# Kernel optimization log

Hardware: AMD Instinct MI355X
Metric: run time of the kernel (lower is better)

## Reference

```python
import jax, jax.numpy as jnp
import numpy as np

N_NODES = 100_000
N_EDGES = 800_000
IN_DIM = 128
OUT_DIM = 128
H = 8
D = OUT_DIM // H  # head dim = 16
SCALE = float(np.sqrt(OUT_DIM / H))


def setup_inputs() -> dict:
    key = jax.random.key(0)
    k1, k2, k3, k4, k5 = jax.random.split(key, 5)
    x = jax.random.normal(k1, (N_NODES, IN_DIM), dtype=jnp.float32)
    i_node = jax.random.randint(k2, (N_EDGES,), 0, N_NODES)
    j_node = jax.random.randint(k3, (N_EDGES,), 0, N_NODES)
    # nn.Linear weights (bias=False): [out_features, in_features]
    Wqkv = jax.random.normal(k4, (3 * OUT_DIM, IN_DIM), dtype=jnp.float32) / np.sqrt(IN_DIM)
    Wprj = jax.random.normal(k5, (OUT_DIM, OUT_DIM), dtype=jnp.float32) / np.sqrt(OUT_DIM)
    return {"x": x, "Wqkv": Wqkv, "Wprj": Wprj, "i_node": i_node, "j_node": j_node}


def reference(x, Wqkv, Wprj, i_node, j_node):
    N = x.shape[0]
    # node_tf_qkv then einops 'n (h d3) -> h n d3'; we keep [N, H, 3D] layout
    qkv = (x @ Wqkv.T).reshape(N, H, 3 * D)
    q, k, v = qkv[..., :D], qkv[..., D:2 * D], qkv[..., 2 * D:]  # chunk(dim=-1)
    q_e = q[i_node]   # [E, H, D] gather target-node queries
    k_e = k[j_node]   # [E, H, D] gather source-node keys
    v_e = v[j_node]   # [E, H, D] gather source-node values
    alpha = (q_e * k_e).sum(-1) / SCALE          # [E, H] per-edge scores
    # segment softmax grouped by target node i_node (torch_geometric softmax)
    m = jax.ops.segment_max(alpha, i_node, num_segments=N)      # [N, H]
    m = jnp.where(jnp.isfinite(m), m, 0.0)                      # nodes with no edges
    ex = jnp.exp(alpha - m[i_node])                             # [E, H]
    denom = jax.ops.segment_sum(ex, i_node, num_segments=N)     # [N, H]
    w = ex / (denom[i_node] + 1e-16)                            # [E, H]
    # scatter-add weighted values back to target nodes
    out = jax.ops.segment_sum(v_e * w[..., None], i_node, num_segments=N)  # [N, H, D]
    out = out.reshape(N, H * D)                  # einops 'h n d -> n (h d)'
    return out @ Wprj.T
```

## Files before the change

kernel.cpp:

```cpp
#include <hip/hip_runtime.h>
#include <hip/hip_bf16.h>
#include <math.h>

#define N_NODES 100000
#define N_EDGES 800000
#define CAP     64

typedef __bf16 bf16x8 __attribute__((ext_vector_type(8)));
typedef float  f32x4  __attribute__((ext_vector_type(4)));

__device__ inline unsigned short f2bf(float f) {
    unsigned u = __float_as_uint(f);
    u += 0x7FFF + ((u >> 16) & 1);
    return (unsigned short)(u >> 16);
}
__device__ inline float bflo(unsigned u) { return __uint_as_float(u << 16); }
__device__ inline float bfhi(unsigned u) { return __uint_as_float(u & 0xFFFF0000u); }
__device__ inline float2 bfpair(unsigned u) { return make_float2(bflo(u), bfhi(u)); }

__global__ __launch_bounds__(256) void cvt_weights(
    const float* __restrict__ wqkv, const float* __restrict__ wprj,
    unsigned short* __restrict__ wqkvbf, unsigned short* __restrict__ wprjbf)
{
    int idx = blockIdx.x * 256 + threadIdx.x;
    if (idx < 12288) {
        int r = idx >> 5, c4 = idx & 31;
        int h = r / 48, rem = r - h * 48;
        int part = rem >> 4, d = rem & 15;
        int nr = part * 128 + h * 16 + d;
        float4 v = ((const float4*)wqkv)[idx];
        ushort4 o;
        o.x = f2bf(v.x); o.y = f2bf(v.y); o.z = f2bf(v.z); o.w = f2bf(v.w);
        ((ushort4*)wqkvbf)[(nr << 5) + c4] = o;
    } else {
        int i = idx - 12288;
        float4 v = ((const float4*)wprj)[i];
        ushort4 o;
        o.x = f2bf(v.x); o.y = f2bf(v.y); o.z = f2bf(v.z); o.w = f2bf(v.w);
        ((ushort4*)wprjbf)[i] = o;
    }
}

template<bool AFP32, bool BF16OUT>
__global__ __launch_bounds__(256) void gemm_mfma(
    const void* __restrict__ Av, int M,
    const unsigned short* __restrict__ B,
    void* __restrict__ C, int Nb)
{
    __shared__ unsigned short As[64][136];
    __shared__ unsigned short Bs[64][136];
    const int t = threadIdx.x;
    const int row0 = blockIdx.x * 64;

    #pragma unroll
    for (int u = 0; u < 4; ++u) {
        int idx = t + u * 256;
        int r = idx >> 4, c = idx & 15;
        int gr = row0 + r;
        if (AFP32) {
            const float* ap = (const float*)Av + (size_t)gr * 128 + c * 8;
            float4 a0 = make_float4(0.f, 0.f, 0.f, 0.f), a1 = a0;
            if (gr < M) { a0 = ((const float4*)ap)[0]; a1 = ((const float4*)ap)[1]; }
            unsigned w0 = (unsigned)f2bf(a0.x) | ((unsigned)f2bf(a0.y) << 16);
            unsigned w1 = (unsigned)f2bf(a0.z) | ((unsigned)f2bf(a0.w) << 16);
            unsigned w2 = (unsigned)f2bf(a1.x) | ((unsigned)f2bf(a1.y) << 16);
            unsigned w3 = (unsigned)f2bf(a1.z) | ((unsigned)f2bf(a1.w) << 16);
            *(uint4*)&As[r][c * 8] = make_uint4(w0, w1, w2, w3);
        } else {
            float4 val = make_float4(0.f, 0.f, 0.f, 0.f);
            if (gr < M)
                val = *(const float4*)((const unsigned short*)Av + (size_t)gr * 128 + c * 8);
            *(float4*)&As[r][c * 8] = val;
        }
    }

    const int wid = t >> 6, lane = t & 63;
    const int wm = wid >> 1, wn = wid & 1;
    const int lrow = lane & 15, kg = lane >> 4;
    const int br = t >> 4, bc = (t & 15) * 8;

    float4 pb[4];
    #pragma unroll
    for (int u = 0; u < 4; ++u)
        pb[u] = *(const float4*)(B + (size_t)(br + u * 16) * 128 + bc);

    const int NT = Nb / 64;
    for (int ct = 0; ct < NT; ++ct) {
        __syncthreads();
        #pragma unroll
        for (int u = 0; u < 4; ++u)
            *(float4*)&Bs[br + u * 16][bc] = pb[u];
        if (ct + 1 < NT) {
            #pragma unroll
            for (int u = 0; u < 4; ++u)
                pb[u] = *(const float4*)(B + (size_t)((ct + 1) * 64 + br + u * 16) * 128 + bc);
        }
        __syncthreads();

        f32x4 acc[2][2] = {};
        #pragma unroll
        for (int ks = 0; ks < 4; ++ks) {
            bf16x8 af[2], bfr[2];
            #pragma unroll
            for (int m = 0; m < 2; ++m)
                af[m] = *(const bf16x8*)&As[wm * 32 + m * 16 + lrow][ks * 32 + kg * 8];
            #pragma unroll
            for (int n = 0; n < 2; ++n)
                bfr[n] = *(const bf16x8*)&Bs[wn * 32 + n * 16 + lrow][ks * 32 + kg * 8];
            #pragma unroll
            for (int m = 0; m < 2; ++m)
                #pragma unroll
                for (int n = 0; n < 2; ++n)
                    acc[m][n] = __builtin_amdgcn_mfma_f32_16x16x32_bf16(
                        af[m], bfr[n], acc[m][n], 0, 0, 0);
        }

        #pragma unroll
        for (int m = 0; m < 2; ++m)
            #pragma unroll
            for (int reg = 0; reg < 4; ++reg) {
                int gr = row0 + wm * 32 + m * 16 + kg * 4 + reg;
                if (gr < M) {
                    #pragma unroll
                    for (int n = 0; n < 2; ++n) {
                        int gc = ct * 64 + wn * 32 + n * 16 + lrow;
                        if (BF16OUT)
                            ((unsigned short*)C)[(size_t)gr * Nb + gc] = f2bf(acc[m][n][reg]);
                        else
                            ((float*)C)[(size_t)gr * Nb + gc] = acc[m][n][reg];
                    }
                }
            }
    }
}

__global__ __launch_bounds__(256) void scatter_cap(
    const int* __restrict__ i_node, const int* __restrict__ j_node,
    unsigned* __restrict__ cnt, int* __restrict__ jlist)
{
    int e = blockIdx.x * 256 + threadIdx.x;
    if (e < N_EDGES) {
        int i = i_node[e];
        unsigned pos = atomicAdd(&cnt[i], 1u);
        jlist[(size_t)i * CAP + pos] = j_node[e] * 384;
    }
}

__global__ __launch_bounds__(256) void node_gather(
    const unsigned short* __restrict__ qkv,
    const unsigned* __restrict__ cnt,
    const int* __restrict__ jlist,
    unsigned short* __restrict__ accum)
{
    int n = blockIdx.x * 4 + (threadIdx.x >> 6);
    if (n >= N_NODES) return;
    int lane = threadIdx.x & 63;
    int slot = lane >> 4, r = lane & 15;

    const uint4 q = *(const uint4*)(qkv + (size_t)n * 384 + r * 8);
    float2 qf[4] = { bfpair(q.x), bfpair(q.y), bfpair(q.z), bfpair(q.w) };

    unsigned deg = cnt[n];
    const int* jrow = jlist + (size_t)n * CAP;

    float2 acc[4] = {};
    float dsum = 0.f;
    for (unsigned it = 0; it < deg; it += 4) {
        unsigned idx = it + (unsigned)slot;
        bool act = idx < deg;
        int jb = jrow[act ? idx : 0];
        const unsigned short* kb = qkv + (size_t)jb + 128 + r * 8;
        uint4 kq = *(const uint4*)kb;
        uint4 vq = *(const uint4*)(kb + 128);
        float2 kf0 = bfpair(kq.x), kf1 = bfpair(kq.y), kf2 = bfpair(kq.z), kf3 = bfpair(kq.w);
        float2 d2 = qf[0] * kf0 + qf[1] * kf1 + qf[2] * kf2 + qf[3] * kf3;
        float ah = d2.x + d2.y;
        ah += __shfl_xor(ah, 1);
        float ex = act ? __expf(ah * 0.25f) : 0.f;
        dsum += ex;
        float2 e2 = make_float2(ex, ex);
        acc[0] += bfpair(vq.x) * e2;
        acc[1] += bfpair(vq.y) * e2;
        acc[2] += bfpair(vq.z) * e2;
        acc[3] += bfpair(vq.w) * e2;
    }

    float* af = (float*)acc;
    #pragma unroll
    for (int off = 16; off < 64; off <<= 1) {
        dsum += __shfl_xor(dsum, off);
        #pragma unroll
        for (int i = 0; i < 8; ++i) af[i] += __shfl_xor(af[i], off);
    }

    if (slot == 0) {
        float rs = 1.0f / (dsum + 1e-16f);
        unsigned o0 = (unsigned)f2bf(acc[0].x * rs) | ((unsigned)f2bf(acc[0].y * rs) << 16);
        unsigned o1 = (unsigned)f2bf(acc[1].x * rs) | ((unsigned)f2bf(acc[1].y * rs) << 16);
        unsigned o2 = (unsigned)f2bf(acc[2].x * rs) | ((unsigned)f2bf(acc[2].y * rs) << 16);
        unsigned o3 = (unsigned)f2bf(acc[3].x * rs) | ((unsigned)f2bf(acc[3].y * rs) << 16);
        *(uint4*)(accum + (size_t)n * 128 + r * 8) = make_uint4(o0, o1, o2, o3);
    }
}

extern "C" void kernel_launch(void* const* d_in, const int* in_sizes, int n_in,
                              void* d_out, int out_size, void* d_ws, size_t ws_size,
                              hipStream_t stream) {
    const float* x      = (const float*)d_in[0];
    const float* Wqkv   = (const float*)d_in[1];
    const float* Wprj   = (const float*)d_in[2];
    const int*   i_node = (const int*)d_in[3];
    const int*   j_node = (const int*)d_in[4];
    float* out = (float*)d_out;

    char* w = (char*)d_ws;
    unsigned short* qkvbf  = (unsigned short*)w;  w += (size_t)N_NODES * 384 * 2;
    unsigned short* accbf  = (unsigned short*)w;  w += (size_t)N_NODES * 128 * 2;
    unsigned short* wqkvbf = (unsigned short*)w;  w += 384 * 128 * 2;
    unsigned short* wprjbf = (unsigned short*)w;  w += 128 * 128 * 2;
    unsigned* cnt = (unsigned*)w;  w += N_NODES * 4;
    int* jlist = (int*)w;

    hipMemsetAsync(cnt, 0, N_NODES * sizeof(unsigned), stream);

    cvt_weights<<<64, 256, 0, stream>>>(Wqkv, Wprj, wqkvbf, wprjbf);

    scatter_cap<<<(N_EDGES + 255) / 256, 256, 0, stream>>>(i_node, j_node, cnt, jlist);

    gemm_mfma<true, true><<<(N_NODES + 63) / 64, 256, 0, stream>>>(
        x, N_NODES, wqkvbf, qkvbf, 384);

    node_gather<<<(N_NODES + 3) / 4, 256, 0, stream>>>(qkvbf, cnt, jlist, accbf);

    gemm_mfma<false, false><<<(N_NODES + 63) / 64, 256, 0, stream>>>(
        accbf, N_NODES, wprjbf, out, 128);
}
```

Before: 315.0 us.

## Fuse output projection GEMM into node gather kernel via shared-memory tile

The per-node attention aggregation now writes its bf16 result into a 64-row shared-memory tile, and the same block then runs the Wprj MFMA projection and writes fp32 output directly. This removes the intermediate accum buffer round trip through global memory and one kernel launch. The gather kernel now processes 16 nodes per wave sequentially with 64-node blocks, giving fewer blocks and less latency hiding for the irregular gathers. The QKV GEMM drops its register prefetch of B tiles in favour of a direct load plus an extra barrier.

```diff
diff --git a/kernel.cpp b/kernel.cpp
--- a/kernel.cpp
+++ b/kernel.cpp
@@ -41,11 +41,10 @@
     }
 }
 
-template<bool AFP32, bool BF16OUT>
-__global__ __launch_bounds__(256) void gemm_mfma(
-    const void* __restrict__ Av, int M,
+__global__ __launch_bounds__(256) void gemm_qkv(
+    const float* __restrict__ A, int M,
     const unsigned short* __restrict__ B,
-    void* __restrict__ C, int Nb)
+    unsigned short* __restrict__ C)
 {
     __shared__ unsigned short As[64][136];
     __shared__ unsigned short Bs[64][136];
@@ -57,43 +56,28 @@
         int idx = t + u * 256;
         int r = idx >> 4, c = idx & 15;
         int gr = row0 + r;
-        if (AFP32) {
-            const float* ap = (const float*)Av + (size_t)gr * 128 + c * 8;
-            float4 a0 = make_float4(0.f, 0.f, 0.f, 0.f), a1 = a0;
-            if (gr < M) { a0 = ((const float4*)ap)[0]; a1 = ((const float4*)ap)[1]; }
-            unsigned w0 = (unsigned)f2bf(a0.x) | ((unsigned)f2bf(a0.y) << 16);
-            unsigned w1 = (unsigned)f2bf(a0.z) | ((unsigned)f2bf(a0.w) << 16);
-            unsigned w2 = (unsigned)f2bf(a1.x) | ((unsigned)f2bf(a1.y) << 16);
-            unsigned w3 = (unsigned)f2bf(a1.z) | ((unsigned)f2bf(a1.w) << 16);
-            *(uint4*)&As[r][c * 8] = make_uint4(w0, w1, w2, w3);
-        } else {
-            float4 val = make_float4(0.f, 0.f, 0.f, 0.f);
-            if (gr < M)
-                val = *(const float4*)((const unsigned short*)Av + (size_t)gr * 128 + c * 8);
-            *(float4*)&As[r][c * 8] = val;
-        }
+        const float* ap = A + (size_t)gr * 128 + c * 8;
+        float4 a0 = make_float4(0.f, 0.f, 0.f, 0.f), a1 = a0;
+        if (gr < M) { a0 = ((const float4*)ap)[0]; a1 = ((const float4*)ap)[1]; }
+        unsigned w0 = (unsigned)f2bf(a0.x) | ((unsigned)f2bf(a0.y) << 16);
+        unsigned w1 = (unsigned)f2bf(a0.z) | ((unsigned)f2bf(a0.w) << 16);
+        unsigned w2 = (unsigned)f2bf(a1.x) | ((unsigned)f2bf(a1.y) << 16);
+        unsigned w3 = (unsigned)f2bf(a1.z) | ((unsigned)f2bf(a1.w) << 16);
+        *(uint4*)&As[r][c * 8] = make_uint4(w0, w1, w2, w3);
     }
 
     const int wid = t >> 6, lane = t & 63;
     const int wm = wid >> 1, wn = wid & 1;
     const int lrow = lane & 15, kg = lane >> 4;
-    const int br = t >> 4, bc = (t & 15) * 8;
-
-    float4 pb[4];
-    #pragma unroll
-    for (int u = 0; u < 4; ++u)
-        pb[u] = *(const float4*)(B + (size_t)(br + u * 16) * 128 + bc);
-
-    const int NT = Nb / 64;
+
+    const int NT = 6;
     for (int ct = 0; ct < NT; ++ct) {
-        __syncthreads();
-        #pragma unroll
-        for (int u = 0; u < 4; ++u)
-            *(float4*)&Bs[br + u * 16][bc] = pb[u];
-        if (ct + 1 < NT) {
-            #pragma unroll
-            for (int u = 0; u < 4; ++u)
-                pb[u] = *(const float4*)(B + (size_t)((ct + 1) * 64 + br + u * 16) * 128 + bc);
+        #pragma unroll
+        for (int u = 0; u < 4; ++u) {
+            int idx = t + u * 256;
+            int r = idx >> 4, c = idx & 15;
+            float4 val = *(const float4*)(B + (size_t)(ct * 64 + r) * 128 + c * 8);
+            *(float4*)&Bs[r][c * 8] = val;
         }
         __syncthreads();
 
@@ -124,13 +108,11 @@
                     #pragma unroll
                     for (int n = 0; n < 2; ++n) {
                         int gc = ct * 64 + wn * 32 + n * 16 + lrow;
-                        if (BF16OUT)
-                            ((unsigned short*)C)[(size_t)gr * Nb + gc] = f2bf(acc[m][n][reg]);
-                        else
-                            ((float*)C)[(size_t)gr * Nb + gc] = acc[m][n][reg];
+                        C[(size_t)gr * 384 + gc] = f2bf(acc[m][n][reg]);
                     }
                 }
             }
+        __syncthreads();
     }
 }
 
@@ -146,60 +128,104 @@
     }
 }
 
-__global__ __launch_bounds__(256) void node_gather(
+__global__ __launch_bounds__(256) void node_gather_proj(
     const unsigned short* __restrict__ qkv,
     const unsigned* __restrict__ cnt,
     const int* __restrict__ jlist,
-    unsigned short* __restrict__ accum)
-{
-    int n = blockIdx.x * 4 + (threadIdx.x >> 6);
-    if (n >= N_NODES) return;
-    int lane = threadIdx.x & 63;
-    int slot = lane >> 4, r = lane & 15;
-
-    const uint4 q = *(const uint4*)(qkv + (size_t)n * 384 + r * 8);
-    float2 qf[4] = { bfpair(q.x), bfpair(q.y), bfpair(q.z), bfpair(q.w) };
-
-    unsigned deg = cnt[n];
-    const int* jrow = jlist + (size_t)n * CAP;
-
-    float2 acc[4] = {};
-    float dsum = 0.f;
-    for (unsigned it = 0; it < deg; it += 4) {
-        unsigned idx = it + (unsigned)slot;
-        bool act = idx < deg;
-        int jb = jrow[act ? idx : 0];
-        const unsigned short* kb = qkv + (size_t)jb + 128 + r * 8;
-        uint4 kq = *(const uint4*)kb;
-        uint4 vq = *(const uint4*)(kb + 128);
-        float2 kf0 = bfpair(kq.x), kf1 = bfpair(kq.y), kf2 = bfpair(kq.z), kf3 = bfpair(kq.w);
-        float2 d2 = qf[0] * kf0 + qf[1] * kf1 + qf[2] * kf2 + qf[3] * kf3;
-        float ah = d2.x + d2.y;
-        ah += __shfl_xor(ah, 1);
-        float ex = act ? __expf(ah * 0.25f) : 0.f;
-        dsum += ex;
-        float2 e2 = make_float2(ex, ex);
-        acc[0] += bfpair(vq.x) * e2;
-        acc[1] += bfpair(vq.y) * e2;
-        acc[2] += bfpair(vq.z) * e2;
-        acc[3] += bfpair(vq.w) * e2;
-    }
-
-    float* af = (float*)acc;
-    #pragma unroll
-    for (int off = 16; off < 64; off <<= 1) {
-        dsum += __shfl_xor(dsum, off);
-        #pragma unroll
-        for (int i = 0; i < 8; ++i) af[i] += __shfl_xor(af[i], off);
-    }
-
-    if (slot == 0) {
-        float rs = 1.0f / (dsum + 1e-16f);
-        unsigned o0 = (unsigned)f2bf(acc[0].x * rs) | ((unsigned)f2bf(acc[0].y * rs) << 16);
-        unsigned o1 = (unsigned)f2bf(acc[1].x * rs) | ((unsigned)f2bf(acc[1].y * rs) << 16);
-        unsigned o2 = (unsigned)f2bf(acc[2].x * rs) | ((unsigned)f2bf(acc[2].y * rs) << 16);
-        unsigned o3 = (unsigned)f2bf(acc[3].x * rs) | ((unsigned)f2bf(acc[3].y * rs) << 16);
-        *(uint4*)(accum + (size_t)n * 128 + r * 8) = make_uint4(o0, o1, o2, o3);
+    const unsigned short* __restrict__ wprj,
+    float* __restrict__ out)
+{
+    __shared__ unsigned short Acc[64 * 136];
+    const int t = threadIdx.x;
+    const int w = t >> 6, lane = t & 63;
+    const int slot = lane >> 4, r = lane & 15;
+    const int base = blockIdx.x * 64;
+
+    for (int k = 0; k < 16; ++k) {
+        int n = base + w * 16 + k;
+        if (n >= N_NODES) break;
+
+        const uint4 q = *(const uint4*)(qkv + (size_t)n * 384 + r * 8);
+        float2 qf[4] = { bfpair(q.x), bfpair(q.y), bfpair(q.z), bfpair(q.w) };
+
+        unsigned deg = cnt[n];
+        const int* jrow = jlist + (size_t)n * CAP;
+
+        float2 acc[4] = {};
+        float dsum = 0.f;
+        for (unsigned it = 0; it < deg; it += 4) {
+            unsigned idx = it + (unsigned)slot;
+            bool act = idx < deg;
+            int jb = jrow[act ? idx : 0];
+            const unsigned short* kb = qkv + (size_t)jb + 128 + r * 8;
+            uint4 kq = *(const uint4*)kb;
+            uint4 vq = *(const uint4*)(kb + 128);
+            float2 kf0 = bfpair(kq.x), kf1 = bfpair(kq.y), kf2 = bfpair(kq.z), kf3 = bfpair(kq.w);
+            float2 d2 = qf[0] * kf0 + qf[1] * kf1 + qf[2] * kf2 + qf[3] * kf3;
+            float ah = d2.x + d2.y;
+            ah += __shfl_xor(ah, 1);
+            float ex = act ? __expf(ah * 0.25f) : 0.f;
+            dsum += ex;
+            float2 e2 = make_float2(ex, ex);
+            acc[0] += bfpair(vq.x) * e2;
+            acc[1] += bfpair(vq.y) * e2;
+            acc[2] += bfpair(vq.z) * e2;
+            acc[3] += bfpair(vq.w) * e2;
+        }
+
+        float* af = (float*)acc;
+        #pragma unroll
+        for (int off = 16; off < 64; off <<= 1) {
+            dsum += __shfl_xor(dsum, off);
+            #pragma unroll
+            for (int i = 0; i < 8; ++i) af[i] += __shfl_xor(af[i], off);
+        }
+
+        if (slot == 0) {
+            float rs = 1.0f / (dsum + 1e-16f);
+            unsigned o0 = (unsigned)f2bf(acc[0].x * rs) | ((unsigned)f2bf(acc[0].y * rs) << 16);
+            unsigned o1 = (unsigned)f2bf(acc[1].x * rs) | ((unsigned)f2bf(acc[1].y * rs) << 16);
+            unsigned o2 = (unsigned)f2bf(acc[2].x * rs) | ((unsigned)f2bf(acc[2].y * rs) << 16);
+            unsigned o3 = (unsigned)f2bf(acc[3].x * rs) | ((unsigned)f2bf(acc[3].y * rs) << 16);
+            *(uint4*)&Acc[(w * 16 + k) * 136 + r * 8] = make_uint4(o0, o1, o2, o3);
+        }
+    }
+    __syncthreads();
+
+    const int wm = w >> 1, wn = w & 1;
+    const int lrow = lane & 15, kg = lane >> 4;
+    for (int ct = 0; ct < 2; ++ct) {
+        f32x4 pacc[2][2] = {};
+        #pragma unroll
+        for (int ks = 0; ks < 4; ++ks) {
+            bf16x8 af2[2], bfr[2];
+            #pragma unroll
+            for (int m = 0; m < 2; ++m)
+                af2[m] = *(const bf16x8*)&Acc[(wm * 32 + m * 16 + lrow) * 136 + ks * 32 + kg * 8];
+            #pragma unroll
+            for (int n2 = 0; n2 < 2; ++n2)
+                bfr[n2] = *(const bf16x8*)(wprj
+                    + (size_t)(ct * 64 + wn * 32 + n2 * 16 + lrow) * 128 + ks * 32 + kg * 8);
+            #pragma unroll
+            for (int m = 0; m < 2; ++m)
+                #pragma unroll
+                for (int n2 = 0; n2 < 2; ++n2)
+                    pacc[m][n2] = __builtin_amdgcn_mfma_f32_16x16x32_bf16(
+                        af2[m], bfr[n2], pacc[m][n2], 0, 0, 0);
+        }
+        #pragma unroll
+        for (int m = 0; m < 2; ++m)
+            #pragma unroll
+            for (int reg = 0; reg < 4; ++reg) {
+                int gr = base + wm * 32 + m * 16 + kg * 4 + reg;
+                if (gr < N_NODES) {
+                    #pragma unroll
+                    for (int n2 = 0; n2 < 2; ++n2) {
+                        int gc = ct * 64 + wn * 32 + n2 * 16 + lrow;
+                        out[(size_t)gr * 128 + gc] = pacc[m][n2][reg];
+                    }
+                }
+            }
     }
 }
 
@@ -215,7 +241,6 @@
 
     char* w = (char*)d_ws;
     unsigned short* qkvbf  = (unsigned short*)w;  w += (size_t)N_NODES * 384 * 2;
-    unsigned short* accbf  = (unsigned short*)w;  w += (size_t)N_NODES * 128 * 2;
     unsigned short* wqkvbf = (unsigned short*)w;  w += 384 * 128 * 2;
     unsigned short* wprjbf = (unsigned short*)w;  w += 128 * 128 * 2;
     unsigned* cnt = (unsigned*)w;  w += N_NODES * 4;
@@ -227,11 +252,8 @@
 
     scatter_cap<<<(N_EDGES + 255) / 256, 256, 0, stream>>>(i_node, j_node, cnt, jlist);
 
-    gemm_mfma<true, true><<<(N_NODES + 63) / 64, 256, 0, stream>>>(
-        x, N_NODES, wqkvbf, qkvbf, 384);
-
-    node_gather<<<(N_NODES + 3) / 4, 256, 0, stream>>>(qkvbf, cnt, jlist, accbf);
-
-    gemm_mfma<false, false><<<(N_NODES + 63) / 64, 256, 0, stream>>>(
-        accbf, N_NODES, wprjbf, out, 128);
-}
+    gemm_qkv<<<(N_NODES + 63) / 64, 256, 0, stream>>>(x, N_NODES, wqkvbf, qkvbf);
+
+    node_gather_proj<<<(N_NODES + 63) / 64, 256, 0, stream>>>(
+        qkvbf, cnt, jlist, wprjbf, out);
+}
```

Result: faster. 302.5 us (-4.0%).
